# Kernel tuning notes

Measured on AMD Instinct MI355X. Metric: run time of the kernel, lower is better.

## Reference

```python
import jax, jax.numpy as jnp
import numpy as np

SOFTMAX_TEMP = 0.01
CART_PIXEL_WIDTH = 256
CART_RESOLUTION = 0.2592


def zn_desc(desc):
    # desc: B x C x N. Zero-mean, unit-std over channel dim (torch.std default ddof=1).
    mean = jnp.mean(desc, axis=1, keepdims=True)
    std = jnp.std(desc, axis=1, keepdims=True, ddof=1)
    return (desc - mean) / std


def compute_2D_from_3D(coords):
    cart_min_range = (CART_PIXEL_WIDTH / 2 - 0.5) * CART_RESOLUTION
    u = (cart_min_range + coords[:, 1]) / CART_RESOLUTION
    v = (cart_min_range - coords[:, 0]) / CART_RESOLUTION
    return jnp.stack([u, v], axis=2)


def setup_inputs() -> dict:
    key = jax.random.key(0)
    B, C, N, H, W = 2, 256, 1024, 256, 256
    ks = jax.random.split(key, 4)
    tgt_coords = jax.random.normal(ks[0], (B, 3, H * W), jnp.float32) * 10.0
    tgt_weights = jax.random.uniform(ks[1], (B, 1, H, W), dtype=jnp.float32)
    src_desc_norm = zn_desc(jax.random.normal(ks[2], (B, C, N), jnp.float32))
    tgt_desc = jax.random.normal(ks[3], (B, C, H, W), jnp.float32)
    return {
        'geometry_img': jnp.zeros((1,), jnp.int32),
        'tgt_coords': tgt_coords,
        'tgt_2D': jnp.zeros((1,), jnp.int32),
        'tgt_weights': tgt_weights,
        'tgt_weights_dense': jnp.zeros((1,), jnp.int32),
        'src_desc_norm': src_desc_norm,
        'tgt_desc': tgt_desc,
        'tgt_desc_dense': jnp.zeros((1,), jnp.int32),
        'cam_calib': jnp.zeros((1,), jnp.int32),
        'window_size': 16,
    }


def reference(geometry_img, tgt_coords, tgt_2D, tgt_weights, tgt_weights_dense,
              src_desc_norm, tgt_desc, tgt_desc_dense, cam_calib, window_size):
    B, C = tgt_desc.shape[0], tgt_desc.shape[1]
    M = tgt_desc.shape[2] * tgt_desc.shape[3]
    N = src_desc_norm.shape[2]

    tgt_desc_flat = tgt_desc.reshape(B, C, M)
    tgt_desc_norm = zn_desc(tgt_desc_flat)

    # B x N x M similarity (ZNCC): src^T @ tgt / C
    match_vals = jnp.einsum('bcn,bcm->bnm', src_desc_norm, tgt_desc_norm) / float(C)
    soft_match_vals = jax.nn.softmax(match_vals / SOFTMAX_TEMP, axis=2)
    max_softmax = jnp.max(soft_match_vals, axis=(1, 2))  # (B,)

    # three weighted sums sharing the same softmax matrix
    pseudo_coords = jnp.einsum('bcm,bnm->bcn', tgt_coords, soft_match_vals)
    pseudo_weights = jnp.einsum('bcm,bnm->bcn', tgt_weights.reshape(B, 1, M), soft_match_vals)
    pseudo_descs = jnp.einsum('bcm,bnm->bcn', tgt_desc_flat, soft_match_vals)          # B x C x N

    pseudo_2D = compute_2D_from_3D(pseudo_coords)  # B x N x 2
    pseudo_descs = zn_desc(pseudo_descs)
    valid_pts = jnp.ones((B, 1, N), jnp.int32)
    return pseudo_coords, pseudo_weights, pseudo_descs, pseudo_2D, valid_pts, max_softmax
```

## Files before the change

kernel.cpp:

```cpp
#include <hip/hip_runtime.h>
#include <hip/hip_bf16.h>

#define Bb   2
#define Cc   256
#define Nn   1024
#define Mm   65536
#define MCn  16
#define VROWS 272
#define MSTEP 32
#define MCHUNK (Mm / MCn)
#define NIT  (MCHUNK / MSTEP)

#define SCL_OFF  0L
#define TMC_OFF  524288L
#define TCM_OFF  67633152L
#define SNC_OFF  138936320L
#define PART_OFF 139984896L
#define ZP_OFF   157810688L
#define PP_OFF   157941760L
#define PS_OFF   PART_OFF
#define PS2_OFF  (PART_OFF + 2097152L)

#define O_COORD 0L
#define O_W     6144L
#define O_DESC  8192L
#define O_P2D   532480L
#define O_VALID 536576L
#define O_MAXSM 538624L

using f32x4 = __attribute__((ext_vector_type(4))) float;
using s16x8 = __attribute__((ext_vector_type(8))) short;

__device__ inline unsigned short f2bf(float x) {
    union { float f; unsigned int u; } v; v.f = x;
    unsigned int r = v.u + 0x7FFFu + ((v.u >> 16) & 1u);
    return (unsigned short)(r >> 16);
}
__device__ inline float bf2f(unsigned short u) {
    union { unsigned int u; float f; } v; v.u = ((unsigned int)u) << 16;
    return v.f;
}
__device__ inline float exp2v(float x) {
    float r; asm("v_exp_f32 %0, %1" : "=v"(r) : "v"(x)); return r;
}
__device__ inline unsigned int cvtpk(float lo, float hi) {
    unsigned int r;
    asm("v_cvt_pk_bf16_f32 %0, %1, %2" : "=v"(r) : "v"(lo), "v"(hi));
    return r;
}

__device__ inline void gld_lds16(const unsigned short* g, unsigned short* l) {
    __builtin_amdgcn_global_load_lds(
        (const __attribute__((address_space(1))) unsigned int*)g,
        (__attribute__((address_space(3))) unsigned int*)l, 16, 0, 0);
}

__global__ void k_prep_tgt(const float* __restrict__ tgt,
                           unsigned short* __restrict__ tmc,
                           unsigned short* __restrict__ tcm,
                           float* __restrict__ ps,
                           float* __restrict__ ps2) {
    __shared__ float lds[64][65];
    __shared__ float sm[4][64], sm2[4][64];
    int b = blockIdx.z, cy = blockIdx.y, c0 = cy * 64;
    long m0 = (long)blockIdx.x * 64;
    int ty = threadIdx.x >> 6, tx = threadIdx.x & 63;
    float s = 0.f, s2 = 0.f;
    #pragma unroll
    for (int k = 0; k < 16; ++k) {
        int ci = 4 * k + ty;
        float v = tgt[((long)b * Cc + c0 + ci) * Mm + m0 + tx];
        lds[ci][tx] = v;
        s += v; s2 += v * v;
        tcm[((long)b * VROWS + c0 + ci) * Mm + m0 + tx] = f2bf(v);
    }
    sm[ty][tx] = s; sm2[ty][tx] = s2;
    __syncthreads();
    #pragma unroll
    for (int k = 0; k < 16; ++k) {
        int mi = 4 * k + ty;
        tmc[((long)b * Mm + m0 + mi) * Cc + c0 + tx] = f2bf(lds[tx][mi]);
    }
    if (ty == 0) {
        long o = ((long)b * 4 + cy) * Mm + m0 + tx;
        ps[o]  = (sm[0][tx] + sm[1][tx]) + (sm[2][tx] + sm[3][tx]);
        ps2[o] = (sm2[0][tx] + sm2[1][tx]) + (sm2[2][tx] + sm2[3][tx]);
    }
}

__global__ void k_stats(const float* __restrict__ ps,
                        const float* __restrict__ ps2,
                        const float* __restrict__ coords,
                        const float* __restrict__ weights,
                        float* __restrict__ scl,
                        unsigned short* __restrict__ tcm) {
    int b = blockIdx.y;
    long m = (long)blockIdx.x * 256 + threadIdx.x;
    float s = 0.f, s2 = 0.f;
    #pragma unroll
    for (int k = 0; k < 4; ++k) {
        long o = ((long)b * 4 + k) * Mm + m;
        s += ps[o]; s2 += ps2[o];
    }
    float var = fmaxf((s2 - s * s * (1.0f / Cc)) * (1.0f / (Cc - 1)), 1e-20f);
    scl[(long)b * Mm + m] = 1.4426950408889634f * rsqrtf(var) * (1.0f / (Cc * 0.01f));
    unsigned short* vrow = tcm + ((long)b * VROWS + 256) * Mm + m;
    #pragma unroll
    for (int i = 0; i < 3; ++i) vrow[(long)i * Mm] = f2bf(coords[((long)b * 3 + i) * Mm + m]);
    vrow[3L * Mm] = f2bf(weights[(long)b * Mm + m]);
    vrow[4L * Mm] = 0x3F80;
    #pragma unroll
    for (int i = 5; i < 16; ++i) vrow[(long)i * Mm] = 0;
}

__global__ void k_prep_src(const float* __restrict__ src, unsigned short* __restrict__ snc) {
    __shared__ float lds[64][65];
    int b = blockIdx.z, c0 = blockIdx.y * 64, n0 = blockIdx.x * 64;
    int ty = threadIdx.x >> 6, tx = threadIdx.x & 63;
    #pragma unroll
    for (int k = 0; k < 16; ++k)
        lds[4 * k + ty][tx] = src[((long)b * Cc + c0 + 4 * k + ty) * Nn + n0 + tx];
    __syncthreads();
    #pragma unroll
    for (int k = 0; k < 16; ++k) {
        int ni = 4 * k + ty;
        snc[((long)b * Nn + n0 + ni) * Cc + c0 + tx] = f2bf(lds[tx][ni]);
    }
}

__global__ __launch_bounds__(256, 1) void k_main(const unsigned short* __restrict__ tmc,
                                                 const unsigned short* __restrict__ tcm,
                                                 const unsigned short* __restrict__ snc,
                                                 const float* __restrict__ scl,
                                                 unsigned short* __restrict__ part,
                                                 float* __restrict__ zp,
                                                 float* __restrict__ pp) {
    __shared__ __align__(16) unsigned short kb0[8192], kb1[8192];
    __shared__ __align__(16) unsigned short vb0[8704], vb1[8704], vb2[8704];
    __shared__ __align__(16) unsigned short pbuf[2][4][2][16][56];

    int w = threadIdx.x >> 6, lane = threadIdx.x & 63;
    int l15 = lane & 15, lg = lane >> 4;
    int b = blockIdx.z, nt = blockIdx.y, mc = blockIdx.x;
    int nb = nt * 128 + w * 32;
    long mbase = (long)mc * MCHUNK;

    s16x8 qf[2][8];
    #pragma unroll
    for (int st = 0; st < 2; ++st) {
        const unsigned short* qp = snc + ((long)b * Nn + nb + st * 16 + l15) * Cc + lg * 8;
        #pragma unroll
        for (int cc = 0; cc < 8; ++cc) qf[st][cc] = *(const s16x8*)(qp + cc * 32);
    }

    f32x4 acc[2][17];
    #pragma unroll
    for (int st = 0; st < 2; ++st)
        #pragma unroll
        for (int t = 0; t < 17; ++t) acc[st][t] = (f32x4){0.f, 0.f, 0.f, 0.f};
    float pmax[2] = {0.f, 0.f};

    const unsigned short* tmcb = tmc + (long)b * Mm * Cc;
    const unsigned short* tcmb = tcm + (long)b * VROWS * (long)Mm;
    const unsigned short* ksrc[4];
    #pragma unroll
    for (int i = 0; i < 4; ++i) {
        int ins = w * 4 + i;
        int row = 2 * ins + (lane >> 5);
        int gs  = (lane & 31) ^ (row & 7);
        ksrc[i] = tmcb + (mbase + row) * Cc + gs * 8;
    }
    const unsigned short* vsrc[5];
    int vj = ((lane & 3) ^ ((lane >> 3) & 3)) * 8;
    #pragma unroll
    for (int i = 0; i < 5; ++i) {
        int ins = (i < 4) ? (w * 4 + i) : 16;
        int row = ins * 16 + (lane >> 2);
        vsrc[i] = tcmb + (long)row * Mm + mbase + vj;
    }

    const float* sclb = scl + (long)b * Mm;

    auto stage = [&](unsigned short* kd, unsigned short* vd) {
        #pragma unroll
        for (int i = 0; i < 4; ++i) gld_lds16(ksrc[i], kd + (w * 4 + i) * 512);
        #pragma unroll
        for (int i = 0; i < 4; ++i) gld_lds16(vsrc[i], vd + (w * 4 + i) * 512);
        if (w == 3) gld_lds16(vsrc[4], vd + 16 * 512);
    };
    auto advance = [&]() {
        #pragma unroll
        for (int i = 0; i < 4; ++i) ksrc[i] += MSTEP * Cc;
        #pragma unroll
        for (int i = 0; i < 5; ++i) vsrc[i] += MSTEP;
    };

    unsigned short *kc = kb0, *kn = kb1;
    unsigned short *vp = vb2, *vc = vb0, *vn = vb1;

    stage(kc, vc);
    advance();
    __syncthreads();

    int ksw = (l15 & 7) << 3;
    int vsw = (lg ^ ((l15 >> 1) & 3)) * 8;

    float4 scA = *(const float4*)(sclb + mbase + lg * 4);
    float4 scB = *(const float4*)(sclb + mbase + 16 + lg * 4);

    for (int s = 0; s < NIT; ++s) {
        if (s + 1 < NIT) { stage(kn, vn); advance(); }
        int sn = (s + 1 < NIT) ? s + 1 : s;
        float4 nA = *(const float4*)(sclb + mbase + (long)sn * MSTEP + lg * 4);
        float4 nB = *(const float4*)(sclb + mbase + (long)sn * MSTEP + 16 + lg * 4);

        unsigned short* pw = &pbuf[s & 1][w][0][0][0];
        #pragma unroll
        for (int t = 0; t < 2; ++t) {
            f32x4 dA = (f32x4){0.f, 0.f, 0.f, 0.f};
            f32x4 dB = (f32x4){0.f, 0.f, 0.f, 0.f};
            const unsigned short* kr = kc + (t * 16 + l15) * Cc;
            #pragma unroll
            for (int cc = 0; cc < 8; ++cc) {
                s16x8 kf = *(const s16x8*)(kr + ((cc * 32 + lg * 8) ^ ksw));
                dA = __builtin_amdgcn_mfma_f32_16x16x32_bf16(kf, qf[0][cc], dA, 0, 0, 0);
                dB = __builtin_amdgcn_mfma_f32_16x16x32_bf16(kf, qf[1][cc], dB, 0, 0, 0);
            }
            float4 sc = t ? scB : scA;
            #pragma unroll
            for (int st = 0; st < 2; ++st) {
                f32x4 d = st ? dB : dA;
                float p0 = exp2v(d.x * sc.x);
                float p1 = exp2v(d.y * sc.y);
                float p2 = exp2v(d.z * sc.z);
                float p3 = exp2v(d.w * sc.w);
                pmax[st] = fmaxf(pmax[st], fmaxf(fmaxf(p0, p1), fmaxf(p2, p3)));
                unsigned long long pk =
                    (unsigned long long)cvtpk(p0, p1) | ((unsigned long long)cvtpk(p2, p3) << 32);
                *(unsigned long long*)(pw + (st * 16 + l15) * 56 + t * 16 + lg * 4) = pk;
            }
        }

        if (s) {
            const unsigned short* pr = &pbuf[(s & 1) ^ 1][w][0][0][0];
            s16x8 pfA = *(const s16x8*)(pr + l15 * 56 + lg * 8);
            s16x8 pfB = *(const s16x8*)(pr + (16 + l15) * 56 + lg * 8);
            #pragma unroll
            for (int t = 0; t < 17; ++t) {
                s16x8 vf = *(const s16x8*)(vp + (t * 16 + l15) * MSTEP + vsw);
                acc[0][t] = __builtin_amdgcn_mfma_f32_16x16x32_bf16(vf, pfA, acc[0][t], 0, 0, 0);
                acc[1][t] = __builtin_amdgcn_mfma_f32_16x16x32_bf16(vf, pfB, acc[1][t], 0, 0, 0);
            }
        }

        scA = nA; scB = nB;
        __syncthreads();
        unsigned short* kt = kc; kc = kn; kn = kt;
        unsigned short* vt = vp; vp = vc; vc = vn; vn = vt;
    }

    {
        const unsigned short* pr = &pbuf[(NIT - 1) & 1][w][0][0][0];
        s16x8 pfA = *(const s16x8*)(pr + l15 * 56 + lg * 8);
        s16x8 pfB = *(const s16x8*)(pr + (16 + l15) * 56 + lg * 8);
        #pragma unroll
        for (int t = 0; t < 17; ++t) {
            s16x8 vf = *(const s16x8*)(vp + (t * 16 + l15) * MSTEP + vsw);
            acc[0][t] = __builtin_amdgcn_mfma_f32_16x16x32_bf16(vf, pfA, acc[0][t], 0, 0, 0);
            acc[1][t] = __builtin_amdgcn_mfma_f32_16x16x32_bf16(vf, pfB, acc[1][t], 0, 0, 0);
        }
    }

    #pragma unroll
    for (int st = 0; st < 2; ++st) {
        float pt = fmaxf(pmax[st], __shfl_xor(pmax[st], 16));
        pt = fmaxf(pt, __shfl_xor(pt, 32));
        long zi = ((long)(b * MCn + mc)) * Nn + nb + st * 16;
        if (lg == 1) zp[zi + l15] = acc[st][16].x;
        if (lane < 16) pp[zi + lane] = pt;
        unsigned short* po = part + (((long)(b * MCn + mc) * Nn) + nb + st * 16 + l15) * VROWS;
        #pragma unroll
        for (int t = 0; t < 17; ++t) {
            f32x4 a = acc[st][t];
            unsigned long long pk =
                (unsigned long long)cvtpk(a.x, a.y) | ((unsigned long long)cvtpk(a.z, a.w) << 32);
            *(unsigned long long*)&po[t * 16 + lg * 4] = pk;
        }
    }
}

__global__ void k_epi(const unsigned short* __restrict__ part,
                      const float* __restrict__ zp,
                      const float* __restrict__ pp,
                      float* __restrict__ out) {
    int w = threadIdx.x >> 6, lane = threadIdx.x & 63;
    int bn = blockIdx.x * 4 + w;
    int b = bn >> 10, n = bn & 1023;

    float Z = 0.f, pm = 0.f;
    #pragma unroll
    for (int mc = 0; mc < MCn; ++mc) {
        long zi = ((long)(b * MCn + mc)) * Nn + n;
        Z += zp[zi];
        pm = fmaxf(pm, pp[zi]);
    }
    float invZ = 1.0f / Z;

    float dv[4], s1 = 0.f, s2 = 0.f;
    #pragma unroll
    for (int k = 0; k < 4; ++k) {
        int c = lane + 64 * k;
        float s = 0.f;
        #pragma unroll
        for (int mc = 0; mc < MCn; ++mc)
            s += bf2f(part[((long)(b * MCn + mc) * Nn + n) * VROWS + c]);
        float d = s * invZ;
        dv[k] = d; s1 += d; s2 += d * d;
    }
    #pragma unroll
    for (int off = 1; off < 64; off <<= 1) { s1 += __shfl_xor(s1, off); s2 += __shfl_xor(s2, off); }
    float mean = s1 * (1.0f / 256.0f);
    float var = fmaxf((s2 - 256.0f * mean * mean) * (1.0f / 255.0f), 1e-20f);
    float istd = 1.0f / sqrtf(var);
    #pragma unroll
    for (int k = 0; k < 4; ++k)
        out[O_DESC + ((long)b * Cc + lane + 64 * k) * Nn + n] = (dv[k] - mean) * istd;

    float ex = 0.f;
    if (lane < 4) {
        int c = 256 + lane;
        #pragma unroll
        for (int mc = 0; mc < MCn; ++mc)
            ex += bf2f(part[((long)(b * MCn + mc) * Nn + n) * VROWS + c]);
        ex *= invZ;
    }
    float pc0 = __shfl(ex, 0), pc1 = __shfl(ex, 1), pc2 = __shfl(ex, 2), wv = __shfl(ex, 3);
    if (lane == 0) {
        out[O_COORD + ((long)b * 3 + 0) * Nn + n] = pc0;
        out[O_COORD + ((long)b * 3 + 1) * Nn + n] = pc1;
        out[O_COORD + ((long)b * 3 + 2) * Nn + n] = pc2;
        out[O_W + (long)b * Nn + n] = wv;
        const float cmin = 33.048f;
        out[O_P2D + ((long)b * Nn + n) * 2 + 0] = (cmin + pc1) * (1.0f / 0.2592f);
        out[O_P2D + ((long)b * Nn + n) * 2 + 1] = (cmin - pc0) * (1.0f / 0.2592f);
        out[O_VALID + (long)b * Nn + n] = 1.0f;
        atomicMax((unsigned int*)out + O_MAXSM + b, __float_as_uint(pm * invZ));
    }
}

extern "C" void kernel_launch(void* const* d_in, const int* in_sizes, int n_in,
                              void* d_out, int out_size, void* d_ws, size_t ws_size,
                              hipStream_t stream) {
    const float* tgt_coords  = (const float*)d_in[1];
    const float* tgt_weights = (const float*)d_in[3];
    const float* src_desc    = (const float*)d_in[5];
    const float* tgt_desc    = (const float*)d_in[6];

    char* ws = (char*)d_ws;
    float* scl           = (float*)(ws + SCL_OFF);
    unsigned short* tmc  = (unsigned short*)(ws + TMC_OFF);
    unsigned short* tcm  = (unsigned short*)(ws + TCM_OFF);
    unsigned short* snc  = (unsigned short*)(ws + SNC_OFF);
    unsigned short* part = (unsigned short*)(ws + PART_OFF);
    float* ps            = (float*)(ws + PS_OFF);
    float* ps2           = (float*)(ws + PS2_OFF);
    float* zp            = (float*)(ws + ZP_OFF);
    float* pp            = (float*)(ws + PP_OFF);
    float* out           = (float*)d_out;

    k_prep_tgt<<<dim3(Mm / 64, Cc / 64, Bb), 256, 0, stream>>>(tgt_desc, tmc, tcm, ps, ps2);
    k_stats<<<dim3(Mm / 256, Bb), 256, 0, stream>>>(ps, ps2, tgt_coords, tgt_weights, scl, tcm);
    k_prep_src<<<dim3(Nn / 64, Cc / 64, Bb), 256, 0, stream>>>(src_desc, snc);
    k_main<<<dim3(MCn, Nn / 128, Bb), 256, 0, stream>>>(tmc, tcm, snc, scl, part, zp, pp);
    hipMemsetAsync((char*)d_out + O_MAXSM * 4, 0, 2 * sizeof(float), stream);
    k_epi<<<dim3((Bb * Nn) / 4), 256, 0, stream>>>(part, zp, pp, out);
}
```

Baseline: 324.9 us.

## Deepen K/V LDS pipeline to four stages with counted vmcnt barriers

```diff
diff --git a/kernel.cpp b/kernel.cpp
--- a/kernel.cpp
+++ b/kernel.cpp
@@ -135,9 +135,9 @@
                                                  unsigned short* __restrict__ part,
                                                  float* __restrict__ zp,
                                                  float* __restrict__ pp) {
-    __shared__ __align__(16) unsigned short kb0[8192], kb1[8192];
-    __shared__ __align__(16) unsigned short vb0[8704], vb1[8704], vb2[8704];
-    __shared__ __align__(16) unsigned short pbuf[2][4][2][16][56];
+    __shared__ __align__(16) unsigned short kb[4][8192];
+    __shared__ __align__(16) unsigned short vb[4][8704];
+    __shared__ __align__(16) unsigned short pbuf[2][4][2][16][40];
 
     int w = threadIdx.x >> 6, lane = threadIdx.x & 63;
     int l15 = lane & 15, lg = lane >> 4;
@@ -181,45 +181,54 @@
 
     const float* sclb = scl + (long)b * Mm;
 
-    auto stage = [&](unsigned short* kd, unsigned short* vd) {
+    auto stage = [&](int d) {
+        unsigned short* kd = kb[d];
+        unsigned short* vd = vb[d];
         #pragma unroll
         for (int i = 0; i < 4; ++i) gld_lds16(ksrc[i], kd + (w * 4 + i) * 512);
         #pragma unroll
         for (int i = 0; i < 4; ++i) gld_lds16(vsrc[i], vd + (w * 4 + i) * 512);
         if (w == 3) gld_lds16(vsrc[4], vd + 16 * 512);
-    };
-    auto advance = [&]() {
         #pragma unroll
         for (int i = 0; i < 4; ++i) ksrc[i] += MSTEP * Cc;
         #pragma unroll
         for (int i = 0; i < 5; ++i) vsrc[i] += MSTEP;
     };
 
-    unsigned short *kc = kb0, *kn = kb1;
-    unsigned short *vp = vb2, *vc = vb0, *vn = vb1;
-
-    stage(kc, vc);
-    advance();
-    __syncthreads();
-
     int ksw = (l15 & 7) << 3;
     int vsw = (lg ^ ((l15 >> 1) & 3)) * 8;
 
+    auto cbar = [&](bool counted) {
+        if (counted) {
+            if (w == 3) asm volatile("s_waitcnt vmcnt(9)" ::: "memory");
+            else        asm volatile("s_waitcnt vmcnt(8)" ::: "memory");
+        } else {
+            asm volatile("s_waitcnt vmcnt(0)" ::: "memory");
+        }
+        __builtin_amdgcn_s_barrier();
+        __builtin_amdgcn_sched_barrier(0);
+    };
+
     float4 scA = *(const float4*)(sclb + mbase + lg * 4);
     float4 scB = *(const float4*)(sclb + mbase + 16 + lg * 4);
+    stage(0);
+    stage(1);
+    cbar(true);
 
     for (int s = 0; s < NIT; ++s) {
-        if (s + 1 < NIT) { stage(kn, vn); advance(); }
         int sn = (s + 1 < NIT) ? s + 1 : s;
         float4 nA = *(const float4*)(sclb + mbase + (long)sn * MSTEP + lg * 4);
         float4 nB = *(const float4*)(sclb + mbase + (long)sn * MSTEP + 16 + lg * 4);
-
+        bool deep = (s + 2 < NIT);
+        if (deep) stage((s + 2) & 3);
+
+        const unsigned short* kbc = kb[s & 3];
         unsigned short* pw = &pbuf[s & 1][w][0][0][0];
         #pragma unroll
         for (int t = 0; t < 2; ++t) {
             f32x4 dA = (f32x4){0.f, 0.f, 0.f, 0.f};
             f32x4 dB = (f32x4){0.f, 0.f, 0.f, 0.f};
-            const unsigned short* kr = kc + (t * 16 + l15) * Cc;
+            const unsigned short* kr = kbc + (t * 16 + l15) * Cc;
             #pragma unroll
             for (int cc = 0; cc < 8; ++cc) {
                 s16x8 kf = *(const s16x8*)(kr + ((cc * 32 + lg * 8) ^ ksw));
@@ -237,35 +246,35 @@
                 pmax[st] = fmaxf(pmax[st], fmaxf(fmaxf(p0, p1), fmaxf(p2, p3)));
                 unsigned long long pk =
                     (unsigned long long)cvtpk(p0, p1) | ((unsigned long long)cvtpk(p2, p3) << 32);
-                *(unsigned long long*)(pw + (st * 16 + l15) * 56 + t * 16 + lg * 4) = pk;
+                *(unsigned long long*)(pw + (st * 16 + l15) * 40 + t * 16 + lg * 4) = pk;
             }
         }
 
         if (s) {
+            const unsigned short* vbc = vb[(s + 3) & 3];
             const unsigned short* pr = &pbuf[(s & 1) ^ 1][w][0][0][0];
-            s16x8 pfA = *(const s16x8*)(pr + l15 * 56 + lg * 8);
-            s16x8 pfB = *(const s16x8*)(pr + (16 + l15) * 56 + lg * 8);
+            s16x8 pfA = *(const s16x8*)(pr + l15 * 40 + lg * 8);
+            s16x8 pfB = *(const s16x8*)(pr + (16 + l15) * 40 + lg * 8);
             #pragma unroll
             for (int t = 0; t < 17; ++t) {
-                s16x8 vf = *(const s16x8*)(vp + (t * 16 + l15) * MSTEP + vsw);
+                s16x8 vf = *(const s16x8*)(vbc + (t * 16 + l15) * MSTEP + vsw);
                 acc[0][t] = __builtin_amdgcn_mfma_f32_16x16x32_bf16(vf, pfA, acc[0][t], 0, 0, 0);
                 acc[1][t] = __builtin_amdgcn_mfma_f32_16x16x32_bf16(vf, pfB, acc[1][t], 0, 0, 0);
             }
         }
 
         scA = nA; scB = nB;
-        __syncthreads();
-        unsigned short* kt = kc; kc = kn; kn = kt;
-        unsigned short* vt = vp; vp = vc; vc = vn; vn = vt;
+        cbar(deep);
     }
 
     {
+        const unsigned short* vbc = vb[(NIT - 1) & 3];
         const unsigned short* pr = &pbuf[(NIT - 1) & 1][w][0][0][0];
-        s16x8 pfA = *(const s16x8*)(pr + l15 * 56 + lg * 8);
-        s16x8 pfB = *(const s16x8*)(pr + (16 + l15) * 56 + lg * 8);
+        s16x8 pfA = *(const s16x8*)(pr + l15 * 40 + lg * 8);
+        s16x8 pfB = *(const s16x8*)(pr + (16 + l15) * 40 + lg * 8);
         #pragma unroll
         for (int t = 0; t < 17; ++t) {
-            s16x8 vf = *(const s16x8*)(vp + (t * 16 + l15) * MSTEP + vsw);
+            s16x8 vf = *(const s16x8*)(vbc + (t * 16 + l15) * MSTEP + vsw);
             acc[0][t] = __builtin_amdgcn_mfma_f32_16x16x32_bf16(vf, pfA, acc[0][t], 0, 0, 0);
             acc[1][t] = __builtin_amdgcn_mfma_f32_16x16x32_bf16(vf, pfB, acc[1][t], 0, 0, 0);
         }
@@ -372,6 +381,6 @@
     k_stats<<<dim3(Mm / 256, Bb), 256, 0, stream>>>(ps, ps2, tgt_coords, tgt_weights, scl, tcm);
     k_prep_src<<<dim3(Nn / 64, Cc / 64, Bb), 256, 0, stream>>>(src_desc, snc);
     k_main<<<dim3(MCn, Nn / 128, Bb), 256, 0, stream>>>(tmc, tcm, snc, scl, part, zp, pp);
-    hipMemsetAsync((char*)d_out + O_MAXSM * 4, 0, 2 * sizeof(float), stream);
+    (void)hipMemsetAsync((char*)d_out + O_MAXSM * 4, 0, 2 * sizeof(float), stream);
     k_epi<<<dim3((Bb * Nn) / 4), 256, 0, stream>>>(part, zp, pp, out);
 }
```

New measurement: 370.4 us. 1.14x slower.
